# Kernel tuning notes

Hardware: AMD Instinct MI355X
Metric: run time of the kernel (lower is better)

The kernel has to match this reference:

```python
import jax, jax.numpy as jnp
import numpy as np

_LAP = jnp.array([[0., 1., 0.], [1., -4., 1.], [0., 1., 0.]], dtype=jnp.float32).reshape(1, 1, 3, 3)  # OIHW

def _laplacian(x):
    # x: [B,1,H,W]; SAME padding (pad=1), stride 1
    return jax.lax.conv_general_dilated(
        x, _LAP, window_strides=(1, 1), padding=((1, 1), (1, 1)),
        dimension_numbers=('NCHW', 'OIHW', 'NCHW'))

def setup_inputs() -> dict:
    key = jax.random.key(0)
    k1, k2 = jax.random.split(key)
    B, C, H, W = 16, 1, 1024, 1024
    pred = jax.random.normal(k1, (B, C, H, W), dtype=jnp.float32)
    target = jax.random.normal(k2, (B, C, H, W), dtype=jnp.float32)
    mask = jnp.ones((B, C, H, W), dtype=jnp.float32)
    return {"pred": pred, "target": target, "mask": mask}

def reference(pred, target, mask):
    # Laplacian curvature of pred and target; note conv is linear so this
    # equals laplacian(pred - target), but we keep the original two-conv math.
    pred_curv = _laplacian(pred)
    target_curv = _laplacian(target)
    loss = jnp.abs(pred_curv - target_curv) * mask
    return loss.sum() / (mask.sum() + 1e-8)
```

## Files before the change

### kernel.cpp

```cpp
#include <hip/hip_runtime.h>


static constexpr int IMG_W = 1024;
static constexpr int IMG_H = 1024;
static constexpr int ROWS  = 8;
static constexpr int NT    = 256;

__global__ __launch_bounds__(NT) void curv_partial_kernel(
    const float* __restrict__ pred,
    const float* __restrict__ target,
    const float* __restrict__ mask,
    float* __restrict__ partial,
    int H)
{
    const int tid  = threadIdx.x;
    const int lane = tid & 63;
    const int blocksPerImage = H / ROWS;
    const int b  = blockIdx.x / blocksPerImage;
    const int y0 = (blockIdx.x % blocksPerImage) * ROWS;
    const size_t imgOff = (size_t)b * H * IMG_W;
    const int x4 = tid * 4;

    auto loadD = [&](int y) -> float4 {
        if (y < 0 || y >= H) return make_float4(0.f, 0.f, 0.f, 0.f);
        const size_t o = imgOff + (size_t)y * IMG_W + x4;
        const float4 p = *reinterpret_cast<const float4*>(pred + o);
        const float4 t = *reinterpret_cast<const float4*>(target + o);
        return make_float4(p.x - t.x, p.y - t.y, p.z - t.z, p.w - t.w);
    };

    float4 d_prev = loadD(y0 - 1);
    float4 d_cur  = loadD(y0);

    float lsum = 0.f, msum = 0.f;

    #pragma unroll
    for (int r = 0; r < ROWS; ++r) {
        const int y = y0 + r;
        const float4 d_next = loadD(y + 1);

        float eL = 0.f, eR = 0.f;
        if (lane == 0 && x4 != 0) {
            const size_t o = imgOff + (size_t)y * IMG_W + (x4 - 1);
            eL = pred[o] - target[o];
        }
        if (lane == 63 && x4 + 4 != IMG_W) {
            const size_t o = imgOff + (size_t)y * IMG_W + (x4 + 4);
            eR = pred[o] - target[o];
        }

        float left  = __shfl_up(d_cur.w, 1, 64);
        float right = __shfl_down(d_cur.x, 1, 64);
        if (lane == 0)  left  = eL;
        if (lane == 63) right = eR;

        const float4 m = *reinterpret_cast<const float4*>(mask + imgOff + (size_t)y * IMG_W + x4);

        const float l0 = d_prev.x + d_next.x + left    + d_cur.y - 4.f * d_cur.x;
        const float l1 = d_prev.y + d_next.y + d_cur.x + d_cur.z - 4.f * d_cur.y;
        const float l2 = d_prev.z + d_next.z + d_cur.y + d_cur.w - 4.f * d_cur.z;
        const float l3 = d_prev.w + d_next.w + d_cur.z + right   - 4.f * d_cur.w;

        lsum += fabsf(l0) * m.x + fabsf(l1) * m.y + fabsf(l2) * m.z + fabsf(l3) * m.w;
        msum += m.x + m.y + m.z + m.w;

        d_prev = d_cur;
        d_cur  = d_next;
    }

    for (int off = 32; off > 0; off >>= 1) {
        lsum += __shfl_down(lsum, off, 64);
        msum += __shfl_down(msum, off, 64);
    }
    __shared__ float wls[NT / 64], wms[NT / 64];
    const int wave = tid >> 6;
    if (lane == 0) { wls[wave] = lsum; wms[wave] = msum; }
    __syncthreads();
    if (tid == 0) {
        float L = 0.f, M = 0.f;
        #pragma unroll
        for (int w = 0; w < NT / 64; ++w) { L += wls[w]; M += wms[w]; }
        partial[2 * (size_t)blockIdx.x]     = L;
        partial[2 * (size_t)blockIdx.x + 1] = M;
    }
}

__global__ __launch_bounds__(256) void curv_final_kernel(
    const float* __restrict__ partial, float* __restrict__ out, int nblocks)
{
    __shared__ float sL[256], sM[256];
    float L = 0.f, M = 0.f;
    for (int i = threadIdx.x; i < nblocks; i += 256) {
        L += partial[2 * (size_t)i];
        M += partial[2 * (size_t)i + 1];
    }
    sL[threadIdx.x] = L; sM[threadIdx.x] = M;
    __syncthreads();
    for (int s = 128; s > 0; s >>= 1) {
        if (threadIdx.x < s) {
            sL[threadIdx.x] += sL[threadIdx.x + s];
            sM[threadIdx.x] += sM[threadIdx.x + s];
        }
        __syncthreads();
    }
    if (threadIdx.x == 0) out[0] = sL[0] / (sM[0] + 1e-8f);
}

extern "C" void kernel_launch(void* const* d_in, const int* in_sizes, int n_in,
                              void* d_out, int out_size, void* d_ws, size_t ws_size,
                              hipStream_t stream) {
    const float* pred   = (const float*)d_in[0];
    const float* target = (const float*)d_in[1];
    const float* mask   = (const float*)d_in[2];
    float* out = (float*)d_out;
    float* partial = (float*)d_ws;

    const int H = IMG_H;
    const int B = in_sizes[0] / (IMG_H * IMG_W);
    const int nblocks = B * (H / ROWS);

    curv_partial_kernel<<<nblocks, NT, 0, stream>>>(pred, target, mask, partial, H);
    curv_final_kernel<<<1, 256, 0, stream>>>(partial, out, nblocks);
}
```

Baseline: 43.56 us.

## Fuse final reduction via atomic ticket, prefetch rows, remap blocks across XCDs

Result: slower. 160.3 us (+268.0%).

```diff
diff --git a/kernel.cpp b/kernel.cpp
--- a/kernel.cpp
+++ b/kernel.cpp
@@ -3,69 +3,92 @@
 
 static constexpr int IMG_W = 1024;
 static constexpr int IMG_H = 1024;
-static constexpr int ROWS  = 8;
+static constexpr int ROWS  = 16;
 static constexpr int NT    = 256;
+static constexpr int NXCD  = 8;
 
-__global__ __launch_bounds__(NT) void curv_partial_kernel(
+__device__ __forceinline__ float4 f4sub(float4 a, float4 b) {
+    return make_float4(a.x - b.x, a.y - b.y, a.z - b.z, a.w - b.w);
+}
+
+__global__ __launch_bounds__(NT, 4) void curv_kernel(
     const float* __restrict__ pred,
     const float* __restrict__ target,
     const float* __restrict__ mask,
     float* __restrict__ partial,
-    int H)
+    unsigned int* __restrict__ counter,
+    float* __restrict__ out,
+    int H, int nblocks)
 {
+    const int bid = blockIdx.x;
+    const int cpx = nblocks / NXCD;
+    const int wid = (bid % NXCD) * cpx + bid / NXCD;
+
     const int tid  = threadIdx.x;
     const int lane = tid & 63;
-    const int blocksPerImage = H / ROWS;
-    const int b  = blockIdx.x / blocksPerImage;
-    const int y0 = (blockIdx.x % blocksPerImage) * ROWS;
-    const size_t imgOff = (size_t)b * H * IMG_W;
+    const int bpi  = H / ROWS;
+    const int img  = wid / bpi;
+    const int y0   = (wid % bpi) * ROWS;
+    const size_t imgOff = (size_t)img * H * IMG_W;
     const int x4 = tid * 4;
 
-    auto loadD = [&](int y) -> float4 {
-        if (y < 0 || y >= H) return make_float4(0.f, 0.f, 0.f, 0.f);
-        const size_t o = imgOff + (size_t)y * IMG_W + x4;
-        const float4 p = *reinterpret_cast<const float4*>(pred + o);
-        const float4 t = *reinterpret_cast<const float4*>(target + o);
-        return make_float4(p.x - t.x, p.y - t.y, p.z - t.z, p.w - t.w);
+    const float4 zero4 = make_float4(0.f, 0.f, 0.f, 0.f);
+    auto raw = [&](const float* __restrict__ p, int y) -> float4 {
+        return (y < 0 || y >= H) ? zero4
+             : *reinterpret_cast<const float4*>(p + imgOff + (size_t)y * IMG_W + x4);
     };
 
-    float4 d_prev = loadD(y0 - 1);
-    float4 d_cur  = loadD(y0);
+    float4 P[2], T[2], M[2];
+    float elP[2], elT[2], erP[2], erT[2];
+
+    auto edgeRaw = [&](int y, int s) {
+        elP[s] = 0.f; elT[s] = 0.f; erP[s] = 0.f; erT[s] = 0.f;
+        if (lane == 0 && x4 != 0) {
+            const size_t o = imgOff + (size_t)y * IMG_W + (x4 - 1);
+            elP[s] = pred[o]; elT[s] = target[o];
+        }
+        if (lane == 63 && x4 + 4 != IMG_W) {
+            const size_t o = imgOff + (size_t)y * IMG_W + (x4 + 4);
+            erP[s] = pred[o]; erT[s] = target[o];
+        }
+    };
+
+    const float4 pA = raw(pred, y0 - 1), tA = raw(target, y0 - 1);
+    const float4 pB = raw(pred, y0),     tB = raw(target, y0);
+    P[0] = raw(pred, y0 + 1); T[0] = raw(target, y0 + 1);
+    P[1] = raw(pred, y0 + 2); T[1] = raw(target, y0 + 2);
+    M[0] = raw(mask, y0);     M[1] = raw(mask, y0 + 1);
+    edgeRaw(y0, 0); edgeRaw(y0 + 1, 1);
+
+    float4 dP = f4sub(pA, tA);
+    float4 dC = f4sub(pB, tB);
 
     float lsum = 0.f, msum = 0.f;
 
     #pragma unroll
     for (int r = 0; r < ROWS; ++r) {
-        const int y = y0 + r;
-        const float4 d_next = loadD(y + 1);
+        const int s = r & 1;
+        const float4 dN = f4sub(P[s], T[s]);
+        const float4 m  = M[s];
 
-        float eL = 0.f, eR = 0.f;
-        if (lane == 0 && x4 != 0) {
-            const size_t o = imgOff + (size_t)y * IMG_W + (x4 - 1);
-            eL = pred[o] - target[o];
-        }
-        if (lane == 63 && x4 + 4 != IMG_W) {
-            const size_t o = imgOff + (size_t)y * IMG_W + (x4 + 4);
-            eR = pred[o] - target[o];
-        }
+        float left  = __shfl_up(dC.w, 1, 64);
+        float right = __shfl_down(dC.x, 1, 64);
+        if (lane == 0)  left  = elP[s] - elT[s];
+        if (lane == 63) right = erP[s] - erT[s];
 
-        float left  = __shfl_up(d_cur.w, 1, 64);
-        float right = __shfl_down(d_cur.x, 1, 64);
-        if (lane == 0)  left  = eL;
-        if (lane == 63) right = eR;
-
-        const float4 m = *reinterpret_cast<const float4*>(mask + imgOff + (size_t)y * IMG_W + x4);
-
-        const float l0 = d_prev.x + d_next.x + left    + d_cur.y - 4.f * d_cur.x;
-        const float l1 = d_prev.y + d_next.y + d_cur.x + d_cur.z - 4.f * d_cur.y;
-        const float l2 = d_prev.z + d_next.z + d_cur.y + d_cur.w - 4.f * d_cur.z;
-        const float l3 = d_prev.w + d_next.w + d_cur.z + right   - 4.f * d_cur.w;
+        const float l0 = dP.x + dN.x + left  + dC.y - 4.f * dC.x;
+        const float l1 = dP.y + dN.y + dC.x  + dC.z - 4.f * dC.y;
+        const float l2 = dP.z + dN.z + dC.y  + dC.w - 4.f * dC.z;
+        const float l3 = dP.w + dN.w + dC.z  + right - 4.f * dC.w;
 
         lsum += fabsf(l0) * m.x + fabsf(l1) * m.y + fabsf(l2) * m.z + fabsf(l3) * m.w;
         msum += m.x + m.y + m.z + m.w;
 
-        d_prev = d_cur;
-        d_cur  = d_next;
+        dP = dC; dC = dN;
+
+        const int y = y0 + r;
+        if (r + 3 <= ROWS) { P[s] = raw(pred, y + 3); T[s] = raw(target, y + 3); }
+        if (r + 2 <  ROWS) { M[s] = raw(mask, y + 2); edgeRaw(y + 2, s); }
     }
 
     for (int off = 32; off > 0; off >>= 1) {
@@ -73,37 +96,41 @@
         msum += __shfl_down(msum, off, 64);
     }
     __shared__ float wls[NT / 64], wms[NT / 64];
+    __shared__ unsigned int s_ticket;
     const int wave = tid >> 6;
     if (lane == 0) { wls[wave] = lsum; wms[wave] = msum; }
     __syncthreads();
     if (tid == 0) {
-        float L = 0.f, M = 0.f;
+        float L = 0.f, Mm = 0.f;
         #pragma unroll
-        for (int w = 0; w < NT / 64; ++w) { L += wls[w]; M += wms[w]; }
-        partial[2 * (size_t)blockIdx.x]     = L;
-        partial[2 * (size_t)blockIdx.x + 1] = M;
+        for (int w = 0; w < NT / 64; ++w) { L += wls[w]; Mm += wms[w]; }
+        __hip_atomic_store(&partial[2 * (size_t)wid],     L,  __ATOMIC_RELAXED, __HIP_MEMORY_SCOPE_AGENT);
+        __hip_atomic_store(&partial[2 * (size_t)wid + 1], Mm, __ATOMIC_RELAXED, __HIP_MEMORY_SCOPE_AGENT);
+        __threadfence();
+        s_ticket = atomicAdd(counter, 1u);
     }
-}
+    __syncthreads();
 
-__global__ __launch_bounds__(256) void curv_final_kernel(
-    const float* __restrict__ partial, float* __restrict__ out, int nblocks)
-{
-    __shared__ float sL[256], sM[256];
-    float L = 0.f, M = 0.f;
-    for (int i = threadIdx.x; i < nblocks; i += 256) {
-        L += partial[2 * (size_t)i];
-        M += partial[2 * (size_t)i + 1];
+    if (s_ticket == (unsigned int)(nblocks - 1)) {
+        __threadfence();
+        float L = 0.f, Mm = 0.f;
+        for (int i = tid; i < nblocks; i += NT) {
+            L  += __hip_atomic_load(&partial[2 * (size_t)i],     __ATOMIC_RELAXED, __HIP_MEMORY_SCOPE_AGENT);
+            Mm += __hip_atomic_load(&partial[2 * (size_t)i + 1], __ATOMIC_RELAXED, __HIP_MEMORY_SCOPE_AGENT);
+        }
+        for (int off = 32; off > 0; off >>= 1) {
+            L  += __shfl_down(L, off, 64);
+            Mm += __shfl_down(Mm, off, 64);
+        }
+        if (lane == 0) { wls[wave] = L; wms[wave] = Mm; }
+        __syncthreads();
+        if (tid == 0) {
+            float LL = 0.f, MM = 0.f;
+            #pragma unroll
+            for (int w = 0; w < NT / 64; ++w) { LL += wls[w]; MM += wms[w]; }
+            out[0] = LL / (MM + 1e-8f);
+        }
     }
-    sL[threadIdx.x] = L; sM[threadIdx.x] = M;
-    __syncthreads();
-    for (int s = 128; s > 0; s >>= 1) {
-        if (threadIdx.x < s) {
-            sL[threadIdx.x] += sL[threadIdx.x + s];
-            sM[threadIdx.x] += sM[threadIdx.x + s];
-        }
-        __syncthreads();
-    }
-    if (threadIdx.x == 0) out[0] = sL[0] / (sM[0] + 1e-8f);
 }
 
 extern "C" void kernel_launch(void* const* d_in, const int* in_sizes, int n_in,
@@ -113,12 +140,14 @@
     const float* target = (const float*)d_in[1];
     const float* mask   = (const float*)d_in[2];
     float* out = (float*)d_out;
-    float* partial = (float*)d_ws;
 
     const int H = IMG_H;
     const int B = in_sizes[0] / (IMG_H * IMG_W);
     const int nblocks = B * (H / ROWS);
 
-    curv_partial_kernel<<<nblocks, NT, 0, stream>>>(pred, target, mask, partial, H);
-    curv_final_kernel<<<1, 256, 0, stream>>>(partial, out, nblocks);
+    float* partial = (float*)d_ws;
+    unsigned int* counter = (unsigned int*)((char*)d_ws + 16384);
+
+    hipMemsetAsync(counter, 0, sizeof(unsigned int), stream);
+    curv_kernel<<<nblocks, NT, 0, stream>>>(pred, target, mask, partial, counter, out, H, nblocks);
 }
```
